# Performance work log

Hardware: AMD Instinct MI355X
Metric: run time of the kernel (lower is better)

Reference implementation:

```python
import jax, jax.numpy as jnp
import numpy as np

N = 12288   # num_nodes
D = 128     # isize
K_TOP = 31  # k + 1, per top_k(similarities, self.k + 1)


def setup_inputs() -> dict:
    key = jax.random.key(0)
    features = jax.random.normal(key, (N, D), dtype=jnp.float32)
    eye = jnp.eye(D, dtype=jnp.float32)  # param_init: weight <- I, bias <- 0
    return {
        "features": features,
        "W1": eye,
        "b1": jnp.zeros((D,), jnp.float32),
        "W2": eye,
        "b2": jnp.zeros((D,), jnp.float32),
    }


def reference(features, W1, b1, W2, b2):
    # internal_forward: Linear -> ReLU -> Linear (nlayers=2, act='relu')
    h = jax.nn.relu(features @ W1.T + b1)
    h = h @ W2.T + b2
    # F.normalize(h, dim=1, p=2) with eps=1e-12
    hn = h / jnp.maximum(jnp.linalg.norm(h, axis=1, keepdims=True), 1e-12)
    # dense N x N cosine similarity
    sim = hn @ hn.T
    # top_k: keep top (k+1) entries per row, zero elsewhere; then apply_non_linearity='relu'
    vals, idx = jax.lax.top_k(sim, K_TOP)          # [N, K_TOP]
    rows = jnp.arange(sim.shape[0])[:, None]       # [N, 1]
    # relu(sim * mask) == scatter relu(top-k values) into a zero matrix
    out = jnp.zeros_like(sim).at[rows, idx].set(jax.nn.relu(vals))
    return out
```

## Files before the change

kernel.cpp:

```cpp
#include <hip/hip_runtime.h>
#include <stdint.h>
#include <math.h>

#define NN 12288
#define DD 128
#define KTOP 31
#define TCAND 64
#define CCAP 128
#define RPB 48
#define WPB 8
#define NIT 48
#define KROW 516

typedef __attribute__((ext_vector_type(8))) short bf16x8;
typedef __attribute__((ext_vector_type(4))) float f32x4;

__device__ __forceinline__ unsigned short f2bf(float x) {
  unsigned int u = __float_as_uint(x);
  u += 0x7fffu + ((u >> 16) & 1u);
  return (unsigned short)(u >> 16);
}

__device__ __forceinline__ unsigned umed3(unsigned a, unsigned b, unsigned c) {
  unsigned d;
  asm("v_med3_u32 %0, %1, %2, %3" : "=v"(d) : "v"(a), "v"(b), "v"(c));
  return d;
}

#define PINS8(Lx, P) { \
  const unsigned p_ = (P); \
  _Pragma("unroll") \
  for (int i_ = 0; i_ < 7; ++i_) \
    Lx[i_] = umed3(p_, Lx[i_], Lx[i_ + 1]); \
  Lx[7] = Lx[7] > p_ ? Lx[7] : p_; }

#define LKEY(ACC, LX, COLBASE) { \
  _Pragma("unroll") \
  for (int r_ = 0; r_ < 4; ++r_) { \
    unsigned bf_ = f2bf((ACC)[r_]); \
    unsigned s_ = (bf_ & 0x8000u) ? 0u : bf_; \
    unsigned p_k = (s_ << 16) | (unsigned)((COLBASE) + quad * 4 + r_); \
    PINS8(LX, p_k) } }

__global__ __launch_bounds__(128)
void wtrans_kernel(const float* __restrict__ W1, const float* __restrict__ W2,
                   float* __restrict__ W1T, float* __restrict__ W2T) {
  const int r = blockIdx.x, c = threadIdx.x;
  W1T[(size_t)c * DD + r] = W1[(size_t)r * DD + c];
  W2T[(size_t)c * DD + r] = W2[(size_t)r * DD + c];
}

__global__ __launch_bounds__(256)
void mlp_norm_kernel(const float* __restrict__ feat,
                     const float* __restrict__ W1T, const float* __restrict__ b1,
                     const float* __restrict__ W2T, const float* __restrict__ b2,
                     double* __restrict__ hn64, unsigned short* __restrict__ hnb) {
  __shared__ double bufA[16][DD];
  __shared__ double bufB[16][DD];
  __shared__ double mnorm[16];
  const int t = threadIdx.x;
  const int c = t & 127;
  const int g = t >> 7;
  const int row0 = blockIdx.x * 16 + g * 8;

  #pragma unroll
  for (int rr = 0; rr < 8; ++rr)
    bufA[g * 8 + rr][c] = (double)feat[(size_t)(row0 + rr) * DD + c];
  __syncthreads();

  {
    double acc[8] = {0,0,0,0,0,0,0,0};
    for (int k = 0; k < DD; k += 2) {
      double w0 = (double)W1T[(size_t)k * DD + c];
      double w1 = (double)W1T[(size_t)(k + 1) * DD + c];
      #pragma unroll
      for (int rr = 0; rr < 8; ++rr) {
        double2 a2 = *(const double2*)(&bufA[g * 8 + rr][k]);
        acc[rr] = fma(w0, a2.x, acc[rr]);
        acc[rr] = fma(w1, a2.y, acc[rr]);
      }
    }
    double bb = (double)b1[c];
    #pragma unroll
    for (int rr = 0; rr < 8; ++rr)
      bufB[g * 8 + rr][c] = fmax(acc[rr] + bb, 0.0);
  }
  __syncthreads();
  {
    double acc[8] = {0,0,0,0,0,0,0,0};
    for (int k = 0; k < DD; k += 2) {
      double w0 = (double)W2T[(size_t)k * DD + c];
      double w1 = (double)W2T[(size_t)(k + 1) * DD + c];
      #pragma unroll
      for (int rr = 0; rr < 8; ++rr) {
        double2 a2 = *(const double2*)(&bufB[g * 8 + rr][k]);
        acc[rr] = fma(w0, a2.x, acc[rr]);
        acc[rr] = fma(w1, a2.y, acc[rr]);
      }
    }
    double bb = (double)b2[c];
    #pragma unroll
    for (int rr = 0; rr < 8; ++rr)
      bufA[g * 8 + rr][c] = acc[rr] + bb;
  }
  __syncthreads();

  const int lane = t & 63;
  const int w = t >> 6;
  #pragma unroll
  for (int r2 = 0; r2 < 4; ++r2) {
    int rr = w * 4 + r2;
    double x0 = bufA[rr][lane];
    double x1 = bufA[rr][lane + 64];
    double s = x0 * x0 + x1 * x1;
    #pragma unroll
    for (int d = 1; d < 64; d <<= 1)
      s += __shfl_xor(s, d);
    if (lane == 0) mnorm[rr] = fmax(sqrt(s), 1e-12);
  }
  __syncthreads();
  #pragma unroll
  for (int rr = 0; rr < 8; ++rr) {
    double v = bufA[g * 8 + rr][c] / mnorm[g * 8 + rr];
    hn64[(size_t)(row0 + rr) * DD + c] = v;
    hnb[(size_t)(row0 + rr) * DD + c] = f2bf((float)v);
  }
}

__global__ __launch_bounds__(512, 2)
void fused_kernel(const unsigned short* __restrict__ hnb,
                  const double* __restrict__ hn64,
                  float* __restrict__ out) {
  __shared__ unsigned keybuf[RPB][KROW];
  __shared__ unsigned scand[WPB][CCAP];
  __shared__ double cres[WPB][CCAP];
  __shared__ float outv[RPB][KTOP];
  __shared__ int   outc[RPB][KTOP];
  const int t = threadIdx.x, lane = t & 63, wv = t >> 6;
  const int m = lane & 15, quad = lane >> 4;
  const int row0 = blockIdx.x * RPB;

  bf16x8 af0[4], af1[4], af2[4];
  #pragma unroll
  for (int kc = 0; kc < 4; ++kc) {
    af0[kc] = *(const bf16x8*)(hnb + (size_t)(row0 + m) * DD + kc * 32 + quad * 8);
    af1[kc] = *(const bf16x8*)(hnb + (size_t)(row0 + 16 + m) * DD + kc * 32 + quad * 8);
    af2[kc] = *(const bf16x8*)(hnb + (size_t)(row0 + 32 + m) * DD + kc * 32 + quad * 8);
  }

  unsigned LA0[8] = {0,0,0,0,0,0,0,0}, LB0[8] = {0,0,0,0,0,0,0,0};
  unsigned LA1[8] = {0,0,0,0,0,0,0,0}, LB1[8] = {0,0,0,0,0,0,0,0};
  unsigned LA2[8] = {0,0,0,0,0,0,0,0}, LB2[8] = {0,0,0,0,0,0,0,0};

  f32x4* outz = (f32x4*)(out + (size_t)row0 * NN);
  const f32x4 z = {0.0f, 0.0f, 0.0f, 0.0f};

  for (int it = 0; it < NIT; ++it) {
    const int cb = it * (WPB * 32) + wv * 32;
    bf16x8 b0[4], b1[4];
    #pragma unroll
    for (int kc = 0; kc < 4; ++kc) {
      b0[kc] = *(const bf16x8*)(hnb + (size_t)(cb + m) * DD + kc * 32 + quad * 8);
      b1[kc] = *(const bf16x8*)(hnb + (size_t)(cb + 16 + m) * DD + kc * 32 + quad * 8);
    }
    f32x4 a00 = {0,0,0,0}, a01 = {0,0,0,0};
    f32x4 a10 = {0,0,0,0}, a11 = {0,0,0,0};
    f32x4 a20 = {0,0,0,0}, a21 = {0,0,0,0};
    #pragma unroll
    for (int kc = 0; kc < 4; ++kc) {
      a00 = __builtin_amdgcn_mfma_f32_16x16x32_bf16(b0[kc], af0[kc], a00, 0, 0, 0);
      a01 = __builtin_amdgcn_mfma_f32_16x16x32_bf16(b1[kc], af0[kc], a01, 0, 0, 0);
      a10 = __builtin_amdgcn_mfma_f32_16x16x32_bf16(b0[kc], af1[kc], a10, 0, 0, 0);
      a11 = __builtin_amdgcn_mfma_f32_16x16x32_bf16(b1[kc], af1[kc], a11, 0, 0, 0);
      a20 = __builtin_amdgcn_mfma_f32_16x16x32_bf16(b0[kc], af2[kc], a20, 0, 0, 0);
      a21 = __builtin_amdgcn_mfma_f32_16x16x32_bf16(b1[kc], af2[kc], a21, 0, 0, 0);
    }
    #pragma unroll
    for (int j = 0; j < 6; ++j)
      __builtin_nontemporal_store(z, &outz[it * 3072 + j * 512 + t]);
    LKEY(a00, LA0, cb)      LKEY(a01, LB0, cb + 16)
    LKEY(a10, LA1, cb)      LKEY(a11, LB1, cb + 16)
    LKEY(a20, LA2, cb)      LKEY(a21, LB2, cb + 16)
  }

  {
    const int sbase = (wv * 4 + quad) * 16;
    unsigned* d0 = &keybuf[m][sbase];
    *(uint4*)(d0)     = make_uint4(LA0[0], LA0[1], LA0[2], LA0[3]);
    *(uint4*)(d0 + 4) = make_uint4(LA0[4], LA0[5], LA0[6], LA0[7]);
    *(uint4*)(d0 + 8) = make_uint4(LB0[0], LB0[1], LB0[2], LB0[3]);
    *(uint4*)(d0 + 12)= make_uint4(LB0[4], LB0[5], LB0[6], LB0[7]);
    unsigned* d1 = &keybuf[16 + m][sbase];
    *(uint4*)(d1)     = make_uint4(LA1[0], LA1[1], LA1[2], LA1[3]);
    *(uint4*)(d1 + 4) = make_uint4(LA1[4], LA1[5], LA1[6], LA1[7]);
    *(uint4*)(d1 + 8) = make_uint4(LB1[0], LB1[1], LB1[2], LB1[3]);
    *(uint4*)(d1 + 12)= make_uint4(LB1[4], LB1[5], LB1[6], LB1[7]);
    unsigned* d2 = &keybuf[32 + m][sbase];
    *(uint4*)(d2)     = make_uint4(LA2[0], LA2[1], LA2[2], LA2[3]);
    *(uint4*)(d2 + 4) = make_uint4(LA2[4], LA2[5], LA2[6], LA2[7]);
    *(uint4*)(d2 + 8) = make_uint4(LB2[0], LB2[1], LB2[2], LB2[3]);
    *(uint4*)(d2 + 12)= make_uint4(LB2[4], LB2[5], LB2[6], LB2[7]);
  }
  __syncthreads();

  for (int ii = 0; ii < 6; ++ii) {
    const int lr = wv * 6 + ii;
    const int grow = row0 + lr;
    unsigned k8[8];
    #pragma unroll
    for (int i = 0; i < 8; ++i)
      k8[i] = keybuf[lr][i * 64 + lane];

    unsigned lo = 0, hi = 0xFFFFu;
    while (lo < hi) {
      unsigned mid = (lo + hi + 1) >> 1;
      int c = 0;
      #pragma unroll
      for (int i = 0; i < 8; ++i) c += (int)((k8[i] >> 16) >= mid);
      #pragma unroll
      for (int d = 1; d < 64; d <<= 1) c += __shfl_xor(c, d);
      if (c >= TCAND) lo = mid; else hi = mid - 1;
    }
    const unsigned thr = lo;

    int cl = 0;
    #pragma unroll
    for (int i = 0; i < 8; ++i) cl += (int)((k8[i] >> 16) >= thr);
    int pre = cl;
    #pragma unroll
    for (int d = 1; d < 64; d <<= 1) {
      int y = __shfl_up(pre, d);
      if (lane >= d) pre += y;
    }
    const int total = __shfl(pre, 63);
    const int nc = total < CCAP ? total : CCAP;
    int slot = pre - cl;
    #pragma unroll
    for (int i = 0; i < 8; ++i) {
      if ((k8[i] >> 16) >= thr) {
        if (slot < CCAP) scand[wv][slot] = k8[i];
        ++slot;
      }
    }

    const double* arow = hn64 + (size_t)grow * DD;
    const int hl = lane >> 5;
    const int kl = (lane & 31) * 4;
    const double a0 = arow[kl], a1 = arow[kl + 1], a2 = arow[kl + 2], a3 = arow[kl + 3];
    const int ng = (nc + 1) >> 1;
    for (int g = 0; g < ng; ++g) {
      const int ci = 2 * g + hl;
      double partial = 0.0;
      if (ci < nc) {
        const int col = (int)(scand[wv][ci] & 0xFFFFu);
        const double* brow = hn64 + (size_t)col * DD + kl;
        double2 b01 = *(const double2*)(brow);
        double2 b23 = *(const double2*)(brow + 2);
        partial = fma(a0, b01.x, fma(a1, b01.y, fma(a2, b23.x, a3 * b23.y)));
      }
      #pragma unroll
      for (int d = 1; d < 32; d <<= 1)
        partial += __shfl_xor(partial, d);
      if ((lane & 31) == 0 && ci < nc) cres[wv][ci] = partial;
    }
    double rv0 = -1.0e300, rv1 = -1.0e300;
    int rc0 = 0x7fffffff, rc1 = 0x7fffffff;
    if (lane < nc)      { rv0 = cres[wv][lane];      rc0 = (int)(scand[wv][lane] & 0xFFFFu); }
    if (lane + 64 < nc) { rv1 = cres[wv][lane + 64]; rc1 = (int)(scand[wv][lane + 64] & 0xFFFFu); }

    for (int itk = 0; itk < KTOP; ++itk) {
      bool f = (rv0 > rv1) || (rv0 == rv1 && rc0 < rc1);
      double bv = f ? rv0 : rv1;
      int bc = f ? rc0 : rc1;
      #pragma unroll
      for (int d = 1; d < 64; d <<= 1) {
        double ov = __shfl_xor(bv, d);
        int    oc = __shfl_xor(bc, d);
        bool tk = (ov > bv) || (ov == bv && oc < bc);
        bv = tk ? ov : bv;
        bc = tk ? oc : bc;
      }
      if (lane == itk) {
        outv[lr][itk] = (float)fmax(bv, 0.0);
        outc[lr][itk] = bc;
      }
      if (rv0 == bv && rc0 == bc) rv0 = -1.0e300;
      else if (rv1 == bv && rc1 == bc) rv1 = -1.0e300;
    }
  }

  asm volatile("s_waitcnt vmcnt(0)" ::: "memory");
  __syncthreads();
  #pragma unroll
  for (int ii = 0; ii < 6; ++ii) {
    const int lr = wv * 6 + ii;
    if (lane < KTOP)
      out[(size_t)(row0 + lr) * NN + outc[lr][lane]] = outv[lr][lane];
  }
}

extern "C" void kernel_launch(void* const* d_in, const int* in_sizes, int n_in,
                              void* d_out, int out_size, void* d_ws, size_t ws_size,
                              hipStream_t stream) {
  const float* feat = (const float*)d_in[0];
  const float* W1 = (const float*)d_in[1];
  const float* b1 = (const float*)d_in[2];
  const float* W2 = (const float*)d_in[3];
  const float* b2 = (const float*)d_in[4];
  float* out = (float*)d_out;

  double* hn64 = (double*)d_ws;
  unsigned short* hnb = (unsigned short*)(hn64 + (size_t)NN * DD);
  float* W1T = (float*)(hnb + (size_t)NN * DD);
  float* W2T = W1T + DD * DD;

  wtrans_kernel<<<DD, DD, 0, stream>>>(W1, W2, W1T, W2T);
  mlp_norm_kernel<<<NN / 16, 256, 0, stream>>>(feat, W1T, b1, W2T, b2, hn64, hnb);
  fused_kernel<<<NN / RPB, 512, 0, stream>>>(hnb, hn64, out);
}
```

Before: 927.7 us.

## Split fused sim/top-k kernel into 1024-thread MFMA sweep and separate select kernel

The fused kernel is split in two. A 1024-thread simloop kernel (16 waves per block) computes bf16 MFMA similarities, zero-fills the output, and writes each row's per-lane candidate keys into the start of that row of the output buffer, using it as scratch instead of LDS. A separate select kernel, one wave per row, reads the 1024 keys back, thresholds, rescores the candidates in double precision, zeroes the scratch region and scatters the top-k. This frees LDS and raises waves per block to improve MFMA occupancy, at the cost of an extra launch and a global round trip for the keys. The MLP kernel also keeps features in a float LDS buffer and unrolls its first loop by four.

New measurement: 910.3 us. About the same (-1.9%).

```diff
diff --git a/kernel.cpp b/kernel.cpp
--- a/kernel.cpp
+++ b/kernel.cpp
@@ -8,9 +8,9 @@
 #define TCAND 64
 #define CCAP 128
 #define RPB 48
-#define WPB 8
-#define NIT 48
-#define KROW 516
+#define WPL 16
+#define NIT 24
+#define KPROW 1024
 
 typedef __attribute__((ext_vector_type(8))) short bf16x8;
 typedef __attribute__((ext_vector_type(4))) float f32x4;
@@ -55,8 +55,9 @@
                      const float* __restrict__ W1T, const float* __restrict__ b1,
                      const float* __restrict__ W2T, const float* __restrict__ b2,
                      double* __restrict__ hn64, unsigned short* __restrict__ hnb) {
-  __shared__ double bufA[16][DD];
+  __shared__ float  bufA[16][DD];
   __shared__ double bufB[16][DD];
+  __shared__ double bufC[16][DD];
   __shared__ double mnorm[16];
   const int t = threadIdx.x;
   const int c = t & 127;
@@ -65,19 +66,23 @@
 
   #pragma unroll
   for (int rr = 0; rr < 8; ++rr)
-    bufA[g * 8 + rr][c] = (double)feat[(size_t)(row0 + rr) * DD + c];
+    bufA[g * 8 + rr][c] = feat[(size_t)(row0 + rr) * DD + c];
   __syncthreads();
 
   {
     double acc[8] = {0,0,0,0,0,0,0,0};
-    for (int k = 0; k < DD; k += 2) {
+    for (int k = 0; k < DD; k += 4) {
       double w0 = (double)W1T[(size_t)k * DD + c];
       double w1 = (double)W1T[(size_t)(k + 1) * DD + c];
+      double w2 = (double)W1T[(size_t)(k + 2) * DD + c];
+      double w3 = (double)W1T[(size_t)(k + 3) * DD + c];
       #pragma unroll
       for (int rr = 0; rr < 8; ++rr) {
-        double2 a2 = *(const double2*)(&bufA[g * 8 + rr][k]);
-        acc[rr] = fma(w0, a2.x, acc[rr]);
-        acc[rr] = fma(w1, a2.y, acc[rr]);
+        f32x4 a4 = *(const f32x4*)(&bufA[g * 8 + rr][k]);
+        acc[rr] = fma(w0, (double)a4.x, acc[rr]);
+        acc[rr] = fma(w1, (double)a4.y, acc[rr]);
+        acc[rr] = fma(w2, (double)a4.z, acc[rr]);
+        acc[rr] = fma(w3, (double)a4.w, acc[rr]);
       }
     }
     double bb = (double)b1[c];
@@ -101,7 +106,7 @@
     double bb = (double)b2[c];
     #pragma unroll
     for (int rr = 0; rr < 8; ++rr)
-      bufA[g * 8 + rr][c] = acc[rr] + bb;
+      bufC[g * 8 + rr][c] = acc[rr] + bb;
   }
   __syncthreads();
 
@@ -110,8 +115,8 @@
   #pragma unroll
   for (int r2 = 0; r2 < 4; ++r2) {
     int rr = w * 4 + r2;
-    double x0 = bufA[rr][lane];
-    double x1 = bufA[rr][lane + 64];
+    double x0 = bufC[rr][lane];
+    double x1 = bufC[rr][lane + 64];
     double s = x0 * x0 + x1 * x1;
     #pragma unroll
     for (int d = 1; d < 64; d <<= 1)
@@ -121,21 +126,15 @@
   __syncthreads();
   #pragma unroll
   for (int rr = 0; rr < 8; ++rr) {
-    double v = bufA[g * 8 + rr][c] / mnorm[g * 8 + rr];
+    double v = bufC[g * 8 + rr][c] / mnorm[g * 8 + rr];
     hn64[(size_t)(row0 + rr) * DD + c] = v;
     hnb[(size_t)(row0 + rr) * DD + c] = f2bf((float)v);
   }
 }
 
-__global__ __launch_bounds__(512, 2)
-void fused_kernel(const unsigned short* __restrict__ hnb,
-                  const double* __restrict__ hn64,
-                  float* __restrict__ out) {
-  __shared__ unsigned keybuf[RPB][KROW];
-  __shared__ unsigned scand[WPB][CCAP];
-  __shared__ double cres[WPB][CCAP];
-  __shared__ float outv[RPB][KTOP];
-  __shared__ int   outc[RPB][KTOP];
+__global__ __launch_bounds__(1024)
+void simloop_kernel(const unsigned short* __restrict__ hnb,
+                    float* __restrict__ out) {
   const int t = threadIdx.x, lane = t & 63, wv = t >> 6;
   const int m = lane & 15, quad = lane >> 4;
   const int row0 = blockIdx.x * RPB;
@@ -156,147 +155,155 @@
   const f32x4 z = {0.0f, 0.0f, 0.0f, 0.0f};
 
   for (int it = 0; it < NIT; ++it) {
-    const int cb = it * (WPB * 32) + wv * 32;
-    bf16x8 b0[4], b1[4];
-    #pragma unroll
-    for (int kc = 0; kc < 4; ++kc) {
-      b0[kc] = *(const bf16x8*)(hnb + (size_t)(cb + m) * DD + kc * 32 + quad * 8);
-      b1[kc] = *(const bf16x8*)(hnb + (size_t)(cb + 16 + m) * DD + kc * 32 + quad * 8);
-    }
+    const int cb = it * (WPL * 32) + wv * 32;
     f32x4 a00 = {0,0,0,0}, a01 = {0,0,0,0};
     f32x4 a10 = {0,0,0,0}, a11 = {0,0,0,0};
     f32x4 a20 = {0,0,0,0}, a21 = {0,0,0,0};
     #pragma unroll
     for (int kc = 0; kc < 4; ++kc) {
-      a00 = __builtin_amdgcn_mfma_f32_16x16x32_bf16(b0[kc], af0[kc], a00, 0, 0, 0);
-      a01 = __builtin_amdgcn_mfma_f32_16x16x32_bf16(b1[kc], af0[kc], a01, 0, 0, 0);
-      a10 = __builtin_amdgcn_mfma_f32_16x16x32_bf16(b0[kc], af1[kc], a10, 0, 0, 0);
-      a11 = __builtin_amdgcn_mfma_f32_16x16x32_bf16(b1[kc], af1[kc], a11, 0, 0, 0);
-      a20 = __builtin_amdgcn_mfma_f32_16x16x32_bf16(b0[kc], af2[kc], a20, 0, 0, 0);
-      a21 = __builtin_amdgcn_mfma_f32_16x16x32_bf16(b1[kc], af2[kc], a21, 0, 0, 0);
+      bf16x8 b0 = *(const bf16x8*)(hnb + (size_t)(cb + m) * DD + kc * 32 + quad * 8);
+      bf16x8 b1 = *(const bf16x8*)(hnb + (size_t)(cb + 16 + m) * DD + kc * 32 + quad * 8);
+      a00 = __builtin_amdgcn_mfma_f32_16x16x32_bf16(b0, af0[kc], a00, 0, 0, 0);
+      a01 = __builtin_amdgcn_mfma_f32_16x16x32_bf16(b1, af0[kc], a01, 0, 0, 0);
+      a10 = __builtin_amdgcn_mfma_f32_16x16x32_bf16(b0, af1[kc], a10, 0, 0, 0);
+      a11 = __builtin_amdgcn_mfma_f32_16x16x32_bf16(b1, af1[kc], a11, 0, 0, 0);
+      a20 = __builtin_amdgcn_mfma_f32_16x16x32_bf16(b0, af2[kc], a20, 0, 0, 0);
+      a21 = __builtin_amdgcn_mfma_f32_16x16x32_bf16(b1, af2[kc], a21, 0, 0, 0);
     }
     #pragma unroll
     for (int j = 0; j < 6; ++j)
-      __builtin_nontemporal_store(z, &outz[it * 3072 + j * 512 + t]);
+      __builtin_nontemporal_store(z, &outz[it * 6144 + j * 1024 + t]);
     LKEY(a00, LA0, cb)      LKEY(a01, LB0, cb + 16)
     LKEY(a10, LA1, cb)      LKEY(a11, LB1, cb + 16)
     LKEY(a20, LA2, cb)      LKEY(a21, LB2, cb + 16)
   }
 
-  {
-    const int sbase = (wv * 4 + quad) * 16;
-    unsigned* d0 = &keybuf[m][sbase];
+  asm volatile("s_waitcnt vmcnt(0)" ::: "memory");
+  __syncthreads();
+
+  const int sbase = (wv * 4 + quad) * 16;
+  {
+    unsigned* d0 = (unsigned*)(out + (size_t)(row0 + m) * NN) + sbase;
     *(uint4*)(d0)     = make_uint4(LA0[0], LA0[1], LA0[2], LA0[3]);
     *(uint4*)(d0 + 4) = make_uint4(LA0[4], LA0[5], LA0[6], LA0[7]);
     *(uint4*)(d0 + 8) = make_uint4(LB0[0], LB0[1], LB0[2], LB0[3]);
     *(uint4*)(d0 + 12)= make_uint4(LB0[4], LB0[5], LB0[6], LB0[7]);
-    unsigned* d1 = &keybuf[16 + m][sbase];
+    unsigned* d1 = (unsigned*)(out + (size_t)(row0 + 16 + m) * NN) + sbase;
     *(uint4*)(d1)     = make_uint4(LA1[0], LA1[1], LA1[2], LA1[3]);
     *(uint4*)(d1 + 4) = make_uint4(LA1[4], LA1[5], LA1[6], LA1[7]);
     *(uint4*)(d1 + 8) = make_uint4(LB1[0], LB1[1], LB1[2], LB1[3]);
     *(uint4*)(d1 + 12)= make_uint4(LB1[4], LB1[5], LB1[6], LB1[7]);
-    unsigned* d2 = &keybuf[32 + m][sbase];
+    unsigned* d2 = (unsigned*)(out + (size_t)(row0 + 32 + m) * NN) + sbase;
     *(uint4*)(d2)     = make_uint4(LA2[0], LA2[1], LA2[2], LA2[3]);
     *(uint4*)(d2 + 4) = make_uint4(LA2[4], LA2[5], LA2[6], LA2[7]);
     *(uint4*)(d2 + 8) = make_uint4(LB2[0], LB2[1], LB2[2], LB2[3]);
     *(uint4*)(d2 + 12)= make_uint4(LB2[4], LB2[5], LB2[6], LB2[7]);
   }
-  __syncthreads();
-
-  for (int ii = 0; ii < 6; ++ii) {
-    const int lr = wv * 6 + ii;
-    const int grow = row0 + lr;
-    unsigned k8[8];
-    #pragma unroll
-    for (int i = 0; i < 8; ++i)
-      k8[i] = keybuf[lr][i * 64 + lane];
-
-    unsigned lo = 0, hi = 0xFFFFu;
-    while (lo < hi) {
-      unsigned mid = (lo + hi + 1) >> 1;
-      int c = 0;
-      #pragma unroll
-      for (int i = 0; i < 8; ++i) c += (int)((k8[i] >> 16) >= mid);
-      #pragma unroll
-      for (int d = 1; d < 64; d <<= 1) c += __shfl_xor(c, d);
-      if (c >= TCAND) lo = mid; else hi = mid - 1;
-    }
-    const unsigned thr = lo;
-
-    int cl = 0;
-    #pragma unroll
-    for (int i = 0; i < 8; ++i) cl += (int)((k8[i] >> 16) >= thr);
-    int pre = cl;
+}
+
+__global__ __launch_bounds__(256)
+void select_kernel(const double* __restrict__ hn64, float* __restrict__ out) {
+  __shared__ unsigned scand[4][CCAP];
+  __shared__ double cres[4][CCAP];
+  const int t = threadIdx.x, lane = t & 63, wv = t >> 6;
+  const int row = blockIdx.x * 4 + wv;
+  float* orow = out + (size_t)row * NN;
+
+  unsigned k16[16];
+  {
+    const unsigned* src = (const unsigned*)orow + lane * 16;
+    #pragma unroll
+    for (int q = 0; q < 4; ++q) {
+      uint4 a = *(const uint4*)(src + q * 4);
+      k16[q * 4 + 0] = a.x; k16[q * 4 + 1] = a.y;
+      k16[q * 4 + 2] = a.z; k16[q * 4 + 3] = a.w;
+    }
+  }
+
+  unsigned lo = 0, hi = 0xFFFFu;
+  while (lo < hi) {
+    unsigned mid = (lo + hi + 1) >> 1;
+    int c = 0;
+    #pragma unroll
+    for (int i = 0; i < 16; ++i) c += (int)((k16[i] >> 16) >= mid);
+    #pragma unroll
+    for (int d = 1; d < 64; d <<= 1) c += __shfl_xor(c, d);
+    if (c >= TCAND) lo = mid; else hi = mid - 1;
+  }
+  const unsigned thr = lo;
+
+  int cl = 0;
+  #pragma unroll
+  for (int i = 0; i < 16; ++i) cl += (int)((k16[i] >> 16) >= thr);
+  int pre = cl;
+  #pragma unroll
+  for (int d = 1; d < 64; d <<= 1) {
+    int y = __shfl_up(pre, d);
+    if (lane >= d) pre += y;
+  }
+  const int total = __shfl(pre, 63);
+  const int nc = total < CCAP ? total : CCAP;
+  int slot = pre - cl;
+  #pragma unroll
+  for (int i = 0; i < 16; ++i) {
+    if ((k16[i] >> 16) >= thr) {
+      if (slot < CCAP) scand[wv][slot] = k16[i];
+      ++slot;
+    }
+  }
+
+  const double* arow = hn64 + (size_t)row * DD;
+  const int hl = lane >> 5;
+  const int kl = (lane & 31) * 4;
+  const double a0 = arow[kl], a1 = arow[kl + 1], a2 = arow[kl + 2], a3 = arow[kl + 3];
+  const int ng = (nc + 1) >> 1;
+  for (int g = 0; g < ng; ++g) {
+    const int ci = 2 * g + hl;
+    double partial = 0.0;
+    if (ci < nc) {
+      const int col = (int)(scand[wv][ci] & 0xFFFFu);
+      const double* brow = hn64 + (size_t)col * DD + kl;
+      double2 b01 = *(const double2*)(brow);
+      double2 b23 = *(const double2*)(brow + 2);
+      partial = fma(a0, b01.x, fma(a1, b01.y, fma(a2, b23.x, a3 * b23.y)));
+    }
+    #pragma unroll
+    for (int d = 1; d < 32; d <<= 1)
+      partial += __shfl_xor(partial, d);
+    if ((lane & 31) == 0 && ci < nc) cres[wv][ci] = partial;
+  }
+  double rv0 = -1.0e300, rv1 = -1.0e300;
+  int rc0 = 0x7fffffff, rc1 = 0x7fffffff;
+  if (lane < nc)      { rv0 = cres[wv][lane];      rc0 = (int)(scand[wv][lane] & 0xFFFFu); }
+  if (lane + 64 < nc) { rv1 = cres[wv][lane + 64]; rc1 = (int)(scand[wv][lane + 64] & 0xFFFFu); }
+
+  float fkv = 0.0f; int fkc = 0;
+  for (int itk = 0; itk < KTOP; ++itk) {
+    bool f = (rv0 > rv1) || (rv0 == rv1 && rc0 < rc1);
+    double bv = f ? rv0 : rv1;
+    int bc = f ? rc0 : rc1;
     #pragma unroll
     for (int d = 1; d < 64; d <<= 1) {
-      int y = __shfl_up(pre, d);
-      if (lane >= d) pre += y;
-    }
-    const int total = __shfl(pre, 63);
-    const int nc = total < CCAP ? total : CCAP;
-    int slot = pre - cl;
-    #pragma unroll
-    for (int i = 0; i < 8; ++i) {
-      if ((k8[i] >> 16) >= thr) {
-        if (slot < CCAP) scand[wv][slot] = k8[i];
-        ++slot;
-      }
-    }
-
-    const double* arow = hn64 + (size_t)grow * DD;
-    const int hl = lane >> 5;
-    const int kl = (lane & 31) * 4;
-    const double a0 = arow[kl], a1 = arow[kl + 1], a2 = arow[kl + 2], a3 = arow[kl + 3];
-    const int ng = (nc + 1) >> 1;
-    for (int g = 0; g < ng; ++g) {
-      const int ci = 2 * g + hl;
-      double partial = 0.0;
-      if (ci < nc) {
-        const int col = (int)(scand[wv][ci] & 0xFFFFu);
-        const double* brow = hn64 + (size_t)col * DD + kl;
-        double2 b01 = *(const double2*)(brow);
-        double2 b23 = *(const double2*)(brow + 2);
-        partial = fma(a0, b01.x, fma(a1, b01.y, fma(a2, b23.x, a3 * b23.y)));
-      }
-      #pragma unroll
-      for (int d = 1; d < 32; d <<= 1)
-        partial += __shfl_xor(partial, d);
-      if ((lane & 31) == 0 && ci < nc) cres[wv][ci] = partial;
-    }
-    double rv0 = -1.0e300, rv1 = -1.0e300;
-    int rc0 = 0x7fffffff, rc1 = 0x7fffffff;
-    if (lane < nc)      { rv0 = cres[wv][lane];      rc0 = (int)(scand[wv][lane] & 0xFFFFu); }
-    if (lane + 64 < nc) { rv1 = cres[wv][lane + 64]; rc1 = (int)(scand[wv][lane + 64] & 0xFFFFu); }
-
-    for (int itk = 0; itk < KTOP; ++itk) {
-      bool f = (rv0 > rv1) || (rv0 == rv1 && rc0 < rc1);
-      double bv = f ? rv0 : rv1;
-      int bc = f ? rc0 : rc1;
-      #pragma unroll
-      for (int d = 1; d < 64; d <<= 1) {
-        double ov = __shfl_xor(bv, d);
-        int    oc = __shfl_xor(bc, d);
-        bool tk = (ov > bv) || (ov == bv && oc < bc);
-        bv = tk ? ov : bv;
-        bc = tk ? oc : bc;
-      }
-      if (lane == itk) {
-        outv[lr][itk] = (float)fmax(bv, 0.0);
-        outc[lr][itk] = bc;
-      }
-      if (rv0 == bv && rc0 == bc) rv0 = -1.0e300;
-      else if (rv1 == bv && rc1 == bc) rv1 = -1.0e300;
-    }
-  }
-
+      double ov = __shfl_xor(bv, d);
+      int    oc = __shfl_xor(bc, d);
+      bool tk = (ov > bv) || (ov == bv && oc < bc);
+      bv = tk ? ov : bv;
+      bc = tk ? oc : bc;
+    }
+    if (lane == itk) { fkv = (float)fmax(bv, 0.0); fkc = bc; }
+    if (rv0 == bv && rc0 == bc) rv0 = -1.0e300;
+    else if (rv1 == bv && rc1 == bc) rv1 = -1.0e300;
+  }
+
+  {
+    f32x4* zp = (f32x4*)orow;
+    const f32x4 z = {0.0f, 0.0f, 0.0f, 0.0f};
+    #pragma unroll
+    for (int j = 0; j < 4; ++j)
+      __builtin_nontemporal_store(z, &zp[j * 64 + lane]);
+  }
   asm volatile("s_waitcnt vmcnt(0)" ::: "memory");
-  __syncthreads();
-  #pragma unroll
-  for (int ii = 0; ii < 6; ++ii) {
-    const int lr = wv * 6 + ii;
-    if (lane < KTOP)
-      out[(size_t)(row0 + lr) * NN + outc[lr][lane]] = outv[lr][lane];
-  }
+  if (lane < KTOP) orow[fkc] = fkv;
 }
 
 extern "C" void kernel_launch(void* const* d_in, const int* in_sizes, int n_in,
@@ -316,5 +323,6 @@
 
   wtrans_kernel<<<DD, DD, 0, stream>>>(W1, W2, W1T, W2T);
   mlp_norm_kernel<<<NN / 16, 256, 0, stream>>>(feat, W1T, b1, W2T, b2, hn64, hnb);
-  fused_kernel<<<NN / RPB, 512, 0, stream>>>(hnb, hn64, out);
-}
+  simloop_kernel<<<NN / RPB, 1024, 0, stream>>>(hnb, out);
+  select_kernel<<<NN / 4, 256, 0, stream>>>(hn64, out);
+}
```
